# Kernel optimization log

Hardware: AMD Instinct MI355X
Metric: run time of the kernel (lower is better)

Reference implementation:

```python
import jax, jax.numpy as jnp
import numpy as np

N = 100000
E = 1600000
D_IN = 128
D_HID = 128
D_OUT = 64


def mish(x):
    return x * jnp.tanh(jax.nn.softplus(x))


def sage_conv(x, src, dst, W_l, b_l, W_r):
    # gather source-node features along edges, mean-aggregate at destination
    msg = x[src]  # [E, d]
    agg = jax.ops.segment_sum(msg, dst, num_segments=N)  # [N, d]
    cnt = jax.ops.segment_sum(jnp.ones((E,), x.dtype), dst, num_segments=N)
    agg = agg / jnp.maximum(cnt, 1.0)[:, None]
    # PyG SAGEConv: lin_l(aggregated) + lin_r(root); lin_r has no bias
    return agg @ W_l.T + b_l + x @ W_r.T


def setup_inputs() -> dict:
    key = jax.random.key(0)
    ks = jax.random.split(key, 10)
    s = lambda d: 1.0 / np.sqrt(d)
    return {
        "x": jax.random.normal(ks[0], (N, D_IN), jnp.float32),
        "edge_index": jax.random.randint(ks[1], (2, E), 0, N, jnp.int64),
        "W_l0": jax.random.normal(ks[2], (D_HID, D_IN), jnp.float32) * s(D_IN),
        "b_l0": jnp.zeros((D_HID,), jnp.float32),
        "W_r0": jax.random.normal(ks[3], (D_HID, D_IN), jnp.float32) * s(D_IN),
        "W_l1": jax.random.normal(ks[4], (D_HID, D_HID), jnp.float32) * s(D_HID),
        "b_l1": jnp.zeros((D_HID,), jnp.float32),
        "W_r1": jax.random.normal(ks[5], (D_HID, D_HID), jnp.float32) * s(D_HID),
        "W_head": jax.random.normal(ks[6], (D_OUT, D_HID), jnp.float32) * s(D_HID),
        "b_head": jnp.zeros((D_OUT,), jnp.float32),
    }


def reference(x, edge_index, W_l0, b_l0, W_r0, W_l1, b_l1, W_r1, W_head, b_head):
    src, dst = edge_index[0], edge_index[1]
    h = mish(sage_conv(x, src, dst, W_l0, b_l0, W_r0))  # dropout is identity in eval
    h = mish(sage_conv(h, src, dst, W_l1, b_l1, W_r1))
    return h @ W_head.T + b_head
```

## Files before the change

### kernel.cpp

```cpp
#include <hip/hip_runtime.h>
#include <math.h>

#define N_NODES 100000
#define N_EDGES 1600000
#define DF      128
#define D_HEAD  64

#define NWIN    128
#define WIN_SZ  782
#define CAP     13312
#define BCH     8192

typedef __attribute__((ext_vector_type(8))) short bf16x8;
typedef __attribute__((ext_vector_type(4))) float f32x4;

static __device__ __forceinline__ float mish_f(float v) {
    float e = __expf(v);
    float q = 1.0f + e;
    float p = q * q;
    float m = v * (p - 1.0f) / (p + 1.0f);
    return (v > 40.0f) ? v : m;
}

static __device__ __forceinline__ unsigned short f2bf(float f) {
    unsigned int u = __builtin_bit_cast(unsigned int, f);
    unsigned int r = (u + 0x7fffu + ((u >> 16) & 1u)) >> 16;
    return (unsigned short)r;
}


#define XB 12500
#define WB 288

__global__ void cvt_kernel(const float* __restrict__ x,
                           const float* __restrict__ Wl0, const float* __restrict__ Wr0,
                           const float* __restrict__ Wl1, const float* __restrict__ Wr1,
                           const float* __restrict__ Wh,
                           unsigned short* __restrict__ xb, unsigned short* __restrict__ wb,
                           int* __restrict__ bucket_cnt) {
    int b = blockIdx.x;
    if (b < XB) {
        int i = b * 256 + threadIdx.x;
        float4 v = ((const float4*)x)[i];
        ushort4 o;
        o.x = f2bf(v.x); o.y = f2bf(v.y); o.z = f2bf(v.z); o.w = f2bf(v.w);
        ((ushort4*)xb)[i] = o;
    } else if (b < XB + WB) {
        int id = (b - XB) * 256 + threadIdx.x;
        if (id < 65536) {
            int seg = id >> 14;
            int r   = id & 16383;
            const float* W = (seg == 0) ? Wl0 : (seg == 1) ? Wr0 : (seg == 2) ? Wl1 : Wr1;
            wb[id] = f2bf(W[r]);
        } else {
            wb[id] = f2bf(Wh[id - 65536]);
        }
    } else {
        if (threadIdx.x < NWIN) bucket_cnt[threadIdx.x] = 0;
    }
}


__global__ __launch_bounds__(256) void bucket_kernel(const int* __restrict__ src,
                                                     const int* __restrict__ dst,
                                                     int* __restrict__ bucket_cnt,
                                                     unsigned int* __restrict__ pairs) {
    __shared__ int cnt[NWIN][4];
    __shared__ int cur[NWIN][4];
    int tid = threadIdx.x;
    int set = tid & 3;
    int e0  = blockIdx.x * BCH;
    for (int i = tid; i < NWIN * 4; i += 256) ((int*)cnt)[i] = 0;
    __syncthreads();

    int dc[BCH / 256];
    #pragma unroll 4
    for (int i = 0; i < BCH / 256; ++i) {
        int e = e0 + tid + i * 256;
        int d = (e < N_EDGES) ? dst[e] : -1;
        dc[i] = d;
        if (d >= 0) atomicAdd(&cnt[d / WIN_SZ][set], 1);
    }
    __syncthreads();
    if (tid < NWIN) {
        int c0 = cnt[tid][0], c1 = cnt[tid][1], c2 = cnt[tid][2], c3 = cnt[tid][3];
        int b = atomicAdd(&bucket_cnt[tid], c0 + c1 + c2 + c3);
        cur[tid][0] = b;
        cur[tid][1] = b + c0;
        cur[tid][2] = b + c0 + c1;
        cur[tid][3] = b + c0 + c1 + c2;
    }
    __syncthreads();
    #pragma unroll 4
    for (int i = 0; i < BCH / 256; ++i) {
        int d = dc[i];
        if (d >= 0) {
            int e  = e0 + tid + i * 256;
            int s  = src[e];
            int w  = d / WIN_SZ;
            int dl = d - w * WIN_SZ;
            int idx = atomicAdd(&cur[w][set], 1);
            if (idx < CAP)
                pairs[(size_t)w * CAP + idx] = (unsigned)s | ((unsigned)dl << 17);
        }
    }
}


__global__ __launch_bounds__(256) void build_win(const unsigned int* __restrict__ pairs,
                                                 const int* __restrict__ bucket_cnt,
                                                 int* __restrict__ rowstart,
                                                 int* __restrict__ csr) {
    __shared__ int ldeg[WIN_SZ];
    __shared__ int lcsr[CAP];
    __shared__ int wsum[4];
    __shared__ int red[4];

    int tid = threadIdx.x;
    int w   = blockIdx.x;
    int base_node = w * WIN_SZ;
    int nn = N_NODES - base_node;
    if (nn > WIN_SZ) nn = WIN_SZ;
    if (nn < 0) nn = 0;

    for (int i = tid; i < WIN_SZ; i += 256) ldeg[i] = 0;

    int val = (tid < w) ? bucket_cnt[tid] : 0;
    #pragma unroll
    for (int o = 32; o; o >>= 1) val += __shfl_xor(val, o);
    if ((tid & 63) == 0) red[tid >> 6] = val;
    int n_pairs = bucket_cnt[w];
    if (n_pairs > CAP) n_pairs = CAP;
    __syncthreads();
    int ebase = red[0] + red[1] + red[2] + red[3];

    const unsigned int* pw = pairs + (size_t)w * CAP;

    for (int i = tid; i < n_pairs; i += 256)
        atomicAdd(&ldeg[pw[i] >> 17], 1);
    __syncthreads();

    int i0 = tid * 4;
    int v[4];
    int s = 0;
    #pragma unroll
    for (int q = 0; q < 4; ++q) {
        v[q] = (i0 + q < nn) ? ldeg[i0 + q] : 0;
        s += v[q];
    }
    int lane = tid & 63, wv = tid >> 6;
    int sc = s;
    #pragma unroll
    for (int d = 1; d < 64; d <<= 1) {
        int t = __shfl_up(sc, d);
        if (lane >= d) sc += t;
    }
    if (lane == 63) wsum[wv] = sc;
    __syncthreads();
    int woff = 0;
    for (int q = 0; q < wv; ++q) woff += wsum[q];
    int run = woff + sc - s;
    #pragma unroll
    for (int q = 0; q < 4; ++q) {
        if (i0 + q < nn) {
            rowstart[base_node + i0 + q] = ebase + run;
            ldeg[i0 + q] = run;
            run += v[q];
        }
    }
    if (w == NWIN - 1 && tid == 0) rowstart[N_NODES] = N_EDGES;
    __syncthreads();

    for (int i = tid; i < n_pairs; i += 256) {
        unsigned int p = pw[i];
        int slot = atomicAdd(&ldeg[p >> 17], 1);
        lcsr[slot] = (int)(p & 0x1FFFFu);
    }
    __syncthreads();

    for (int i = tid; i < n_pairs; i += 256)
        csr[ebase + i] = lcsr[i];
}


__global__ __launch_bounds__(256) void aggregate_kernel(const unsigned short* __restrict__ X,
                                                        const int* __restrict__ rowstart,
                                                        const int* __restrict__ csr,
                                                        unsigned short* __restrict__ out) {
    int wv   = threadIdx.x >> 6;
    int lane = threadIdx.x & 63;
    int node = blockIdx.x * 4 + wv;
    if (node >= N_NODES) return;
    int slot = lane >> 4;
    int l16  = lane & 15;
    int rs0 = rowstart[node];
    int rs1 = rowstart[node + 1];

    float acc[8];
    #pragma unroll
    for (int i = 0; i < 8; ++i) acc[i] = 0.f;

    for (int e0 = rs0; e0 < rs1; e0 += 16) {
        uint4 v[4];
        #pragma unroll
        for (int j = 0; j < 4; ++j) {
            int e = e0 + 4 * j + slot;
            uint4 t = {0u, 0u, 0u, 0u};
            if (e < rs1) t = *(const uint4*)(X + (size_t)csr[e] * DF + l16 * 8);
            v[j] = t;
        }
        #pragma unroll
        for (int j = 0; j < 4; ++j) {
            unsigned int w0[4] = {v[j].x, v[j].y, v[j].z, v[j].w};
            #pragma unroll
            for (int i = 0; i < 4; ++i) {
                acc[2 * i]     += __builtin_bit_cast(float, w0[i] << 16);
                acc[2 * i + 1] += __builtin_bit_cast(float, w0[i] & 0xffff0000u);
            }
        }
    }

    #pragma unroll
    for (int i = 0; i < 8; ++i) {
        acc[i] += __shfl_xor(acc[i], 32);
        acc[i] += __shfl_xor(acc[i], 16);
    }

    int d = rs1 - rs0;
    float inv = 1.0f / (float)(d > 0 ? d : 1);
    if (slot == 0) {
        unsigned int r[4];
        #pragma unroll
        for (int i = 0; i < 4; ++i) {
            unsigned int lo = f2bf(acc[2 * i] * inv);
            unsigned int hi = f2bf(acc[2 * i + 1] * inv);
            r[i] = lo | (hi << 16);
        }
        uint4 o = {r[0], r[1], r[2], r[3]};
        *(uint4*)(out + (size_t)node * DF + l16 * 8) = o;
    }
}


template <int COLS, bool TWO, bool MISH, bool OUT_BF16>
__global__ __launch_bounds__(256, 3) void sage_gemm(const unsigned short* __restrict__ A,
                                                    const unsigned short* __restrict__ H,
                                                    const unsigned short* __restrict__ Wl,
                                                    const unsigned short* __restrict__ Wr,
                                                    const float* __restrict__ bias,
                                                    void* __restrict__ out) {
    constexpr int NT  = COLS / 16;
    constexpr int LDA = 136;
    __shared__ unsigned short Ws[COLS * LDA];

    int tid  = threadIdx.x;
    int wv   = tid >> 6;
    int lane = tid & 63;
    int quad = lane >> 4;
    int l16  = lane & 15;
    int m0   = blockIdx.x * 128;

    int arow0 = m0 + wv * 32 + l16;
    int arow1 = arow0 + 16;
    if (arow0 > N_NODES - 1) arow0 = N_NODES - 1;
    if (arow1 > N_NODES - 1) arow1 = N_NODES - 1;

    f32x4 acc[2][NT];
    #pragma unroll
    for (int t = 0; t < 2; ++t)
        #pragma unroll
        for (int n = 0; n < NT; ++n) acc[t][n] = (f32x4){0.f, 0.f, 0.f, 0.f};

    #pragma unroll
    for (int phase = 0; phase < (TWO ? 2 : 1); ++phase) {
        const unsigned short* Ain = phase ? H : A;
        const unsigned short* Win = phase ? Wr : Wl;
        if (phase) __syncthreads();
        #pragma unroll
        for (int i = 0; i < COLS / 16; ++i) {
            int idx = tid + i * 256;
            int r   = idx >> 4;
            int cb  = (idx & 15) * 8;
            *(uint4*)&Ws[r * LDA + cb] = *(const uint4*)&Win[r * 128 + cb];
        }
        __syncthreads();

        const unsigned short* Ap0 = Ain + (size_t)arow0 * 128 + quad * 8;
        const unsigned short* Ap1 = Ain + (size_t)arow1 * 128 + quad * 8;
        #pragma unroll
        for (int ks = 0; ks < 4; ++ks) {
            bf16x8 af0 = *(const bf16x8*)(Ap0 + ks * 32);
            bf16x8 af1 = *(const bf16x8*)(Ap1 + ks * 32);
            #pragma unroll
            for (int n = 0; n < NT; ++n) {
                bf16x8 bfr = *(const bf16x8*)&Ws[(n * 16 + l16) * LDA + ks * 32 + quad * 8];
                acc[0][n] = __builtin_amdgcn_mfma_f32_16x16x32_bf16(af0, bfr, acc[0][n], 0, 0, 0);
                acc[1][n] = __builtin_amdgcn_mfma_f32_16x16x32_bf16(af1, bfr, acc[1][n], 0, 0, 0);
            }
        }
    }

    #pragma unroll
    for (int t = 0; t < 2; ++t) {
        #pragma unroll
        for (int n = 0; n < NT; ++n) {
            int col = n * 16 + l16;
            float b = bias[col];
            #pragma unroll
            for (int r = 0; r < 4; ++r) {
                int row = m0 + wv * 32 + t * 16 + quad * 4 + r;
                if (row < N_NODES) {
                    float v = acc[t][n][r] + b;
                    if constexpr (MISH) v = mish_f(v);
                    if constexpr (OUT_BF16)
                        ((unsigned short*)out)[(size_t)row * COLS + col] = f2bf(v);
                    else
                        ((float*)out)[(size_t)row * COLS + col] = v;
                }
            }
        }
    }
}


extern "C" void kernel_launch(void* const* d_in, const int* in_sizes, int n_in,
                              void* d_out, int out_size, void* d_ws, size_t ws_size,
                              hipStream_t stream) {
    const float* x   = (const float*)d_in[0];
    const int*   ei  = (const int*)d_in[1];
    const float* Wl0 = (const float*)d_in[2];
    const float* bl0 = (const float*)d_in[3];
    const float* Wr0 = (const float*)d_in[4];
    const float* Wl1 = (const float*)d_in[5];
    const float* bl1 = (const float*)d_in[6];
    const float* Wr1 = (const float*)d_in[7];
    const float* Wh  = (const float*)d_in[8];
    const float* bh  = (const float*)d_in[9];
    float* out = (float*)d_out;

    const int* src = ei;
    const int* dst = ei + N_EDGES;

    char* ws = (char*)d_ws;
    size_t off = 0;
    auto alloc = [&](size_t bytes) -> void* {
        void* p = ws + off;
        off += (bytes + 255) & ~(size_t)255;
        return p;
    };
    int* rowstart   = (int*)alloc((N_NODES + 1) * 4);
    int* csr        = (int*)alloc(N_EDGES * 4);
    int* bucket_cnt = (int*)alloc(NWIN * 4);

    unsigned short* Wb  = (unsigned short*)alloc((size_t)(65536 + 8192) * 2);
    unsigned short* Xb  = (unsigned short*)alloc((size_t)N_NODES * DF * 2);
    unsigned short* Ab  = (unsigned short*)alloc((size_t)N_NODES * DF * 2);
    unsigned short* H1b = (unsigned short*)alloc((size_t)N_NODES * DF * 2);

    unsigned short* Wlb0 = Wb;
    unsigned short* Wrb0 = Wb + 16384;
    unsigned short* Wlb1 = Wb + 32768;
    unsigned short* Wrb1 = Wb + 49152;
    unsigned short* Whb  = Wb + 65536;
    unsigned short* H2b  = Xb;
    unsigned int* pairs  = (unsigned int*)H1b;

    cvt_kernel<<<XB + WB + 1, 256, 0, stream>>>(x, Wl0, Wr0, Wl1, Wr1, Wh, Xb, Wb, bucket_cnt);

    bucket_kernel<<<(N_EDGES + BCH - 1) / BCH, 256, 0, stream>>>(src, dst, bucket_cnt, pairs);
    build_win<<<NWIN, 256, 0, stream>>>(pairs, bucket_cnt, rowstart, csr);

    const int grid = (N_NODES + 127) / 128;

    aggregate_kernel<<<N_NODES / 4, 256, 0, stream>>>(Xb, rowstart, csr, Ab);
    sage_gemm<128, true, true, true><<<grid, 256, 0, stream>>>(Ab, Xb, Wlb0, Wrb0, bl0, H1b);
    aggregate_kernel<<<N_NODES / 4, 256, 0, stream>>>(H1b, rowstart, csr, Ab);
    sage_gemm<128, true, true, true><<<grid, 256, 0, stream>>>(Ab, H1b, Wlb1, Wrb1, bl1, H2b);
    sage_gemm<64, false, false, false><<<grid, 256, 0, stream>>>(H2b, nullptr, Whb, nullptr, bh, out);
}
```

Baseline: 356.9 us.

## Fuse neighbor aggregation, SAGE GEMMs and head projection into per-layer kernels

Replaces separate aggregation and GEMM kernels with one fused kernel per layer. Each block aggregates 128 nodes into shared memory, then runs both MFMA GEMMs; the second layer also applies the head projection in-kernel. This removes the intermediate aggregated-feature buffer round trip and several launches. In exchange, the gather runs serially per wave over 32 nodes with far fewer blocks and lower occupancy, which may reduce latency hiding for the irregular loads.

```diff
diff --git a/kernel.cpp b/kernel.cpp
--- a/kernel.cpp
+++ b/kernel.cpp
@@ -183,75 +183,19 @@
 }
 
 
-__global__ __launch_bounds__(256) void aggregate_kernel(const unsigned short* __restrict__ X,
-                                                        const int* __restrict__ rowstart,
-                                                        const int* __restrict__ csr,
-                                                        unsigned short* __restrict__ out) {
-    int wv   = threadIdx.x >> 6;
-    int lane = threadIdx.x & 63;
-    int node = blockIdx.x * 4 + wv;
-    if (node >= N_NODES) return;
-    int slot = lane >> 4;
-    int l16  = lane & 15;
-    int rs0 = rowstart[node];
-    int rs1 = rowstart[node + 1];
-
-    float acc[8];
-    #pragma unroll
-    for (int i = 0; i < 8; ++i) acc[i] = 0.f;
-
-    for (int e0 = rs0; e0 < rs1; e0 += 16) {
-        uint4 v[4];
-        #pragma unroll
-        for (int j = 0; j < 4; ++j) {
-            int e = e0 + 4 * j + slot;
-            uint4 t = {0u, 0u, 0u, 0u};
-            if (e < rs1) t = *(const uint4*)(X + (size_t)csr[e] * DF + l16 * 8);
-            v[j] = t;
-        }
-        #pragma unroll
-        for (int j = 0; j < 4; ++j) {
-            unsigned int w0[4] = {v[j].x, v[j].y, v[j].z, v[j].w};
-            #pragma unroll
-            for (int i = 0; i < 4; ++i) {
-                acc[2 * i]     += __builtin_bit_cast(float, w0[i] << 16);
-                acc[2 * i + 1] += __builtin_bit_cast(float, w0[i] & 0xffff0000u);
-            }
-        }
-    }
-
-    #pragma unroll
-    for (int i = 0; i < 8; ++i) {
-        acc[i] += __shfl_xor(acc[i], 32);
-        acc[i] += __shfl_xor(acc[i], 16);
-    }
-
-    int d = rs1 - rs0;
-    float inv = 1.0f / (float)(d > 0 ? d : 1);
-    if (slot == 0) {
-        unsigned int r[4];
-        #pragma unroll
-        for (int i = 0; i < 4; ++i) {
-            unsigned int lo = f2bf(acc[2 * i] * inv);
-            unsigned int hi = f2bf(acc[2 * i + 1] * inv);
-            r[i] = lo | (hi << 16);
-        }
-        uint4 o = {r[0], r[1], r[2], r[3]};
-        *(uint4*)(out + (size_t)node * DF + l16 * 8) = o;
-    }
-}
-
-
-template <int COLS, bool TWO, bool MISH, bool OUT_BF16>
-__global__ __launch_bounds__(256, 3) void sage_gemm(const unsigned short* __restrict__ A,
-                                                    const unsigned short* __restrict__ H,
-                                                    const unsigned short* __restrict__ Wl,
-                                                    const unsigned short* __restrict__ Wr,
-                                                    const float* __restrict__ bias,
-                                                    void* __restrict__ out) {
-    constexpr int NT  = COLS / 16;
+template <bool LAYER1>
+__global__ __launch_bounds__(256, 2) void sage_fused(const unsigned short* __restrict__ X,
+                                                     const int* __restrict__ rowstart,
+                                                     const int* __restrict__ csr,
+                                                     const unsigned short* __restrict__ Wl,
+                                                     const unsigned short* __restrict__ Wr,
+                                                     const float* __restrict__ bias,
+                                                     const unsigned short* __restrict__ Wh,
+                                                     const float* __restrict__ bh,
+                                                     void* __restrict__ out) {
     constexpr int LDA = 136;
-    __shared__ unsigned short Ws[COLS * LDA];
+    __shared__ unsigned short At[128 * LDA];
+    __shared__ unsigned short Ws[128 * LDA];
 
     int tid  = threadIdx.x;
     int wv   = tid >> 6;
@@ -260,62 +204,182 @@
     int l16  = lane & 15;
     int m0   = blockIdx.x * 128;
 
-    int arow0 = m0 + wv * 32 + l16;
-    int arow1 = arow0 + 16;
-    if (arow0 > N_NODES - 1) arow0 = N_NODES - 1;
-    if (arow1 > N_NODES - 1) arow1 = N_NODES - 1;
-
-    f32x4 acc[2][NT];
+    #pragma unroll 1
+    for (int nn = 0; nn < 32; ++nn) {
+        int node = m0 + wv * 32 + nn;
+        if (node > N_NODES - 1) node = N_NODES - 1;
+        int rs0 = rowstart[node];
+        int rs1 = rowstart[node + 1];
+
+        float acc[8];
+        #pragma unroll
+        for (int i = 0; i < 8; ++i) acc[i] = 0.f;
+
+        for (int e0 = rs0; e0 < rs1; e0 += 16) {
+            uint4 v[4];
+            #pragma unroll
+            for (int j = 0; j < 4; ++j) {
+                int e = e0 + 4 * j + quad;
+                uint4 t = {0u, 0u, 0u, 0u};
+                if (e < rs1) t = *(const uint4*)(X + (size_t)csr[e] * DF + l16 * 8);
+                v[j] = t;
+            }
+            #pragma unroll
+            for (int j = 0; j < 4; ++j) {
+                unsigned int w0[4] = {v[j].x, v[j].y, v[j].z, v[j].w};
+                #pragma unroll
+                for (int i = 0; i < 4; ++i) {
+                    acc[2 * i]     += __builtin_bit_cast(float, w0[i] << 16);
+                    acc[2 * i + 1] += __builtin_bit_cast(float, w0[i] & 0xffff0000u);
+                }
+            }
+        }
+        #pragma unroll
+        for (int i = 0; i < 8; ++i) {
+            acc[i] += __shfl_xor(acc[i], 32);
+            acc[i] += __shfl_xor(acc[i], 16);
+        }
+        int d = rs1 - rs0;
+        float inv = 1.0f / (float)(d > 0 ? d : 1);
+        if (quad == 0) {
+            unsigned int r[4];
+            #pragma unroll
+            for (int i = 0; i < 4; ++i) {
+                unsigned int lo = f2bf(acc[2 * i] * inv);
+                unsigned int hi = f2bf(acc[2 * i + 1] * inv);
+                r[i] = lo | (hi << 16);
+            }
+            uint4 o = {r[0], r[1], r[2], r[3]};
+            *(uint4*)&At[(wv * 32 + nn) * LDA + l16 * 8] = o;
+        }
+    }
+
+    f32x4 acc0[2][8];
     #pragma unroll
     for (int t = 0; t < 2; ++t)
         #pragma unroll
-        for (int n = 0; n < NT; ++n) acc[t][n] = (f32x4){0.f, 0.f, 0.f, 0.f};
-
-    #pragma unroll
-    for (int phase = 0; phase < (TWO ? 2 : 1); ++phase) {
-        const unsigned short* Ain = phase ? H : A;
-        const unsigned short* Win = phase ? Wr : Wl;
-        if (phase) __syncthreads();
-        #pragma unroll
-        for (int i = 0; i < COLS / 16; ++i) {
+        for (int n = 0; n < 8; ++n) acc0[t][n] = (f32x4){0.f, 0.f, 0.f, 0.f};
+
+    #pragma unroll
+    for (int i = 0; i < 8; ++i) {
+        int idx = tid + i * 256;
+        int r   = idx >> 4;
+        int cb  = (idx & 15) * 8;
+        *(uint4*)&Ws[r * LDA + cb] = *(const uint4*)&Wl[r * 128 + cb];
+    }
+    __syncthreads();
+    {
+        int ar0 = wv * 32 + l16;
+        #pragma unroll
+        for (int ks = 0; ks < 4; ++ks) {
+            bf16x8 af0 = *(const bf16x8*)&At[ar0 * LDA + ks * 32 + quad * 8];
+            bf16x8 af1 = *(const bf16x8*)&At[(ar0 + 16) * LDA + ks * 32 + quad * 8];
+            #pragma unroll
+            for (int n = 0; n < 8; ++n) {
+                bf16x8 bfr = *(const bf16x8*)&Ws[(n * 16 + l16) * LDA + ks * 32 + quad * 8];
+                acc0[0][n] = __builtin_amdgcn_mfma_f32_16x16x32_bf16(af0, bfr, acc0[0][n], 0, 0, 0);
+                acc0[1][n] = __builtin_amdgcn_mfma_f32_16x16x32_bf16(af1, bfr, acc0[1][n], 0, 0, 0);
+            }
+        }
+    }
+    __syncthreads();
+
+    #pragma unroll
+    for (int i = 0; i < 8; ++i) {
+        int idx = tid + i * 256;
+        int r   = idx >> 4;
+        int cb  = (idx & 15) * 8;
+        *(uint4*)&Ws[r * LDA + cb] = *(const uint4*)&Wr[r * 128 + cb];
+    }
+    __syncthreads();
+    {
+        int grow0 = m0 + wv * 32 + l16;
+        int grow1 = grow0 + 16;
+        if (grow0 > N_NODES - 1) grow0 = N_NODES - 1;
+        if (grow1 > N_NODES - 1) grow1 = N_NODES - 1;
+        const unsigned short* Hp0 = X + (size_t)grow0 * DF + quad * 8;
+        const unsigned short* Hp1 = X + (size_t)grow1 * DF + quad * 8;
+        #pragma unroll
+        for (int ks = 0; ks < 4; ++ks) {
+            bf16x8 af0 = *(const bf16x8*)(Hp0 + ks * 32);
+            bf16x8 af1 = *(const bf16x8*)(Hp1 + ks * 32);
+            #pragma unroll
+            for (int n = 0; n < 8; ++n) {
+                bf16x8 bfr = *(const bf16x8*)&Ws[(n * 16 + l16) * LDA + ks * 32 + quad * 8];
+                acc0[0][n] = __builtin_amdgcn_mfma_f32_16x16x32_bf16(af0, bfr, acc0[0][n], 0, 0, 0);
+                acc0[1][n] = __builtin_amdgcn_mfma_f32_16x16x32_bf16(af1, bfr, acc0[1][n], 0, 0, 0);
+            }
+        }
+    }
+
+    if constexpr (!LAYER1) {
+        #pragma unroll
+        for (int t = 0; t < 2; ++t) {
+            #pragma unroll
+            for (int n = 0; n < 8; ++n) {
+                int col = n * 16 + l16;
+                float b = bias[col];
+                #pragma unroll
+                for (int r = 0; r < 4; ++r) {
+                    int row = m0 + wv * 32 + t * 16 + quad * 4 + r;
+                    if (row < N_NODES)
+                        ((unsigned short*)out)[(size_t)row * DF + col] = f2bf(mish_f(acc0[t][n][r] + b));
+                }
+            }
+        }
+    } else {
+        #pragma unroll
+        for (int t = 0; t < 2; ++t) {
+            #pragma unroll
+            for (int n = 0; n < 8; ++n) {
+                int col = n * 16 + l16;
+                float b = bias[col];
+                #pragma unroll
+                for (int r = 0; r < 4; ++r) {
+                    int row = wv * 32 + t * 16 + quad * 4 + r;
+                    At[row * LDA + col] = f2bf(mish_f(acc0[t][n][r] + b));
+                }
+            }
+        }
+        __syncthreads();
+        #pragma unroll
+        for (int i = 0; i < 4; ++i) {
             int idx = tid + i * 256;
             int r   = idx >> 4;
             int cb  = (idx & 15) * 8;
-            *(uint4*)&Ws[r * LDA + cb] = *(const uint4*)&Win[r * 128 + cb];
+            *(uint4*)&Ws[r * LDA + cb] = *(const uint4*)&Wh[r * 128 + cb];
         }
         __syncthreads();
 
-        const unsigned short* Ap0 = Ain + (size_t)arow0 * 128 + quad * 8;
-        const unsigned short* Ap1 = Ain + (size_t)arow1 * 128 + quad * 8;
+        f32x4 acc2[2][4];
+        #pragma unroll
+        for (int t = 0; t < 2; ++t)
+            #pragma unroll
+            for (int n = 0; n < 4; ++n) acc2[t][n] = (f32x4){0.f, 0.f, 0.f, 0.f};
+
+        int ar0 = wv * 32 + l16;
         #pragma unroll
         for (int ks = 0; ks < 4; ++ks) {
-            bf16x8 af0 = *(const bf16x8*)(Ap0 + ks * 32);
-            bf16x8 af1 = *(const bf16x8*)(Ap1 + ks * 32);
-            #pragma unroll
-            for (int n = 0; n < NT; ++n) {
+            bf16x8 af0 = *(const bf16x8*)&At[ar0 * LDA + ks * 32 + quad * 8];
+            bf16x8 af1 = *(const bf16x8*)&At[(ar0 + 16) * LDA + ks * 32 + quad * 8];
+            #pragma unroll
+            for (int n = 0; n < 4; ++n) {
                 bf16x8 bfr = *(const bf16x8*)&Ws[(n * 16 + l16) * LDA + ks * 32 + quad * 8];
-                acc[0][n] = __builtin_amdgcn_mfma_f32_16x16x32_bf16(af0, bfr, acc[0][n], 0, 0, 0);
-                acc[1][n] = __builtin_amdgcn_mfma_f32_16x16x32_bf16(af1, bfr, acc[1][n], 0, 0, 0);
-            }
-        }
-    }
-
-    #pragma unroll
-    for (int t = 0; t < 2; ++t) {
-        #pragma unroll
-        for (int n = 0; n < NT; ++n) {
-            int col = n * 16 + l16;
-            float b = bias[col];
-            #pragma unroll
-            for (int r = 0; r < 4; ++r) {
-                int row = m0 + wv * 32 + t * 16 + quad * 4 + r;
-                if (row < N_NODES) {
-                    float v = acc[t][n][r] + b;
-                    if constexpr (MISH) v = mish_f(v);
-                    if constexpr (OUT_BF16)
-                        ((unsigned short*)out)[(size_t)row * COLS + col] = f2bf(v);
-                    else
-                        ((float*)out)[(size_t)row * COLS + col] = v;
+                acc2[0][n] = __builtin_amdgcn_mfma_f32_16x16x32_bf16(af0, bfr, acc2[0][n], 0, 0, 0);
+                acc2[1][n] = __builtin_amdgcn_mfma_f32_16x16x32_bf16(af1, bfr, acc2[1][n], 0, 0, 0);
+            }
+        }
+        #pragma unroll
+        for (int t = 0; t < 2; ++t) {
+            #pragma unroll
+            for (int n = 0; n < 4; ++n) {
+                int col = n * 16 + l16;
+                float b = bh[col];
+                #pragma unroll
+                for (int r = 0; r < 4; ++r) {
+                    int row = m0 + wv * 32 + t * 16 + quad * 4 + r;
+                    if (row < N_NODES)
+                        ((float*)out)[(size_t)row * D_HEAD + col] = acc2[t][n][r] + b;
                 }
             }
         }
@@ -354,7 +418,6 @@
 
     unsigned short* Wb  = (unsigned short*)alloc((size_t)(65536 + 8192) * 2);
     unsigned short* Xb  = (unsigned short*)alloc((size_t)N_NODES * DF * 2);
-    unsigned short* Ab  = (unsigned short*)alloc((size_t)N_NODES * DF * 2);
     unsigned short* H1b = (unsigned short*)alloc((size_t)N_NODES * DF * 2);
 
     unsigned short* Wlb0 = Wb;
@@ -362,7 +425,6 @@
     unsigned short* Wlb1 = Wb + 32768;
     unsigned short* Wrb1 = Wb + 49152;
     unsigned short* Whb  = Wb + 65536;
-    unsigned short* H2b  = Xb;
     unsigned int* pairs  = (unsigned int*)H1b;
 
     cvt_kernel<<<XB + WB + 1, 256, 0, stream>>>(x, Wl0, Wr0, Wl1, Wr1, Wh, Xb, Wb, bucket_cnt);
@@ -372,9 +434,8 @@
 
     const int grid = (N_NODES + 127) / 128;
 
-    aggregate_kernel<<<N_NODES / 4, 256, 0, stream>>>(Xb, rowstart, csr, Ab);
-    sage_gemm<128, true, true, true><<<grid, 256, 0, stream>>>(Ab, Xb, Wlb0, Wrb0, bl0, H1b);
-    aggregate_kernel<<<N_NODES / 4, 256, 0, stream>>>(H1b, rowstart, csr, Ab);
-    sage_gemm<128, true, true, true><<<grid, 256, 0, stream>>>(Ab, H1b, Wlb1, Wrb1, bl1, H2b);
-    sage_gemm<64, false, false, false><<<grid, 256, 0, stream>>>(H2b, nullptr, Whb, nullptr, bh, out);
-}
+    sage_fused<false><<<grid, 256, 0, stream>>>(Xb, rowstart, csr, Wlb0, Wrb0, bl0,
+                                                nullptr, nullptr, H1b);
+    sage_fused<true><<<grid, 256, 0, stream>>>(H1b, rowstart, csr, Wlb1, Wrb1, bl1,
+                                               Whb, bh, out);
+}
```

Result: slower. 564.5 us (+58.2%).
